# Performance work log

Hardware: AMD Instinct MI355X
Metric: run time of the kernel (lower is better)

Reference implementation:

```python
import jax, jax.numpy as jnp
import numpy as np

ROPE_BASE = 10000.0


def _rope_tables(m, d, dtype):
    # theta_i = 10000 ** (-2*(i-1)/d), i = 0..d/2-1 (faithful to the source's i-1)
    i = jnp.arange(d // 2, dtype=jnp.float32)
    theta = ROPE_BASE ** (-2.0 * (i - 1.0) / d)
    ang = jnp.arange(m, dtype=jnp.float32)[:, None] * theta[None, :]  # [m, d/2]
    return jnp.cos(ang).astype(dtype), jnp.sin(ang).astype(dtype)


def _rope(x, cos, sin):
    # x: [..., m, d]; row-vector times rotation matrix R[pos]:
    # out_2i = x_2i*cos + x_{2i+1}*sin ; out_{2i+1} = -x_2i*sin + x_{2i+1}*cos
    xp = x.reshape(x.shape[:-1] + (x.shape[-1] // 2, 2))
    xe, xo = xp[..., 0], xp[..., 1]
    oe = xe * cos + xo * sin
    oo = -xe * sin + xo * cos
    return jnp.stack([oe, oo], axis=-1).reshape(x.shape)


def setup_inputs() -> dict:
    key = jax.random.key(0)
    ks = jax.random.split(key, 6)
    B, M, D, H = 4, 2048, 512, 8
    s = 0.02
    return {
        "x": jax.random.normal(ks[0], (B, M, D), jnp.float32),
        "wq": jax.random.normal(ks[1], (H, D, D), jnp.float32) * s,
        "wk": jax.random.normal(ks[2], (H, D, D), jnp.float32) * s,
        "wv": jax.random.normal(ks[3], (H, D, D), jnp.float32) * s,
        "w_out": jax.random.normal(ks[4], (D, H * D), jnp.float32) * s,
        "b_out": jnp.zeros((D,), jnp.float32),
    }


def reference(x, wq, wk, wv, w_out, b_out):
    B, M, D = x.shape
    H = wq.shape[0]
    cos, sin = _rope_tables(M, D, x.dtype)
    # per-head projections (torch Linear: y = x @ W.T)
    q = jnp.einsum('bmd,hed->bhme', x, wq)
    k = jnp.einsum('bmd,hed->bhme', x, wk)
    v = jnp.einsum('bmd,hed->bhme', x, wv)
    qr = _rope(q, cos, sin)
    kr = _rope(k, cos, sin)
    scale = 1.0 / jnp.sqrt(jnp.asarray(D, x.dtype))
    scores = jnp.einsum('bhme,bhne->bhmn', qr, kr) * scale
    causal = jnp.tril(jnp.ones((M, M), bool))
    scores = jnp.where(causal, scores, jnp.asarray(-jnp.inf, scores.dtype))
    attn = jax.nn.softmax(scores, axis=-1)
    o = jnp.einsum('bhmn,bhne->bhme', attn, v)
    # concat heads on last dim (head order preserved), then output linear
    o = o.transpose(0, 2, 1, 3).reshape(B, M, H * D)
    y = jnp.einsum('bmf,df->bmd', o, w_out) + b_out
    return y  # dropout is identity in eval mode
```

## Files before the change

kernel.cpp:

```cpp
#include <hip/hip_runtime.h>
#include <hip/hip_bf16.h>
#include <math.h>


typedef __attribute__((ext_vector_type(8))) __bf16 bf16x8;
typedef __attribute__((ext_vector_type(4))) __bf16 bf16x4;
typedef __attribute__((ext_vector_type(4))) float f32x4;

#define MFMA16(a, b, c) __builtin_amdgcn_mfma_f32_16x16x32_bf16((a), (b), (c), 0, 0, 0)

__device__ __forceinline__ void g2l16(const void* g, void* l) {
  __builtin_amdgcn_global_load_lds((const __attribute__((address_space(1))) void*)g,
                                   (__attribute__((address_space(3))) void*)l, 16, 0, 0);
}

__global__ void prep_k(const float* __restrict__ x, const float* __restrict__ wq,
                       const float* __restrict__ wk, const float* __restrict__ wv,
                       const float* __restrict__ wo,
                       __bf16* __restrict__ xb, __bf16* __restrict__ wqb,
                       __bf16* __restrict__ wkb, __bf16* __restrict__ wvb,
                       __bf16* __restrict__ wob,
                       float* __restrict__ ct, float* __restrict__ st) {
  int i = blockIdx.x * 256 + threadIdx.x;
  if (i < 3145728) {
    const float* src;
    __bf16* dst;
    int off = i;
    if (i < 1048576) { src = x; dst = xb; }
    else if (i < 1572864) { src = wq; dst = wqb; off = i - 1048576; }
    else if (i < 2097152) { src = wk; dst = wkb; off = i - 1572864; }
    else if (i < 2621440) { src = wv; dst = wvb; off = i - 2097152; }
    else { src = wo; dst = wob; off = i - 2621440; }
    float4 f = reinterpret_cast<const float4*>(src)[off];
    bf16x4 o;
    o.x = (__bf16)f.x; o.y = (__bf16)f.y; o.z = (__bf16)f.z; o.w = (__bf16)f.w;
    reinterpret_cast<bf16x4*>(dst)[off] = o;
  } else {
    int idx = i - 3145728;
    int m = idx >> 8, j = idx & 255;
    float e = (-2.0f * ((float)j - 1.0f) / 512.0f) * 13.287712379549449f;
    float theta = exp2f(e);
    float ang = (float)m * theta;
    float s, c;
    sincosf(ang, &s, &c);
    ct[idx] = c;
    st[idx] = s;
  }
}

__global__ __launch_bounds__(256, 2) void qkv_gemm_k(
    const __bf16* __restrict__ Xb,
    const __bf16* __restrict__ Wqb, const __bf16* __restrict__ Wkb, const __bf16* __restrict__ Wvb,
    const float* __restrict__ ct, const float* __restrict__ st,
    __bf16* __restrict__ Q, __bf16* __restrict__ K, __bf16* __restrict__ VT,
    int G, int lg, int h0) {
  const int z = blockIdx.z;
  const int which = z >> lg, hl = z & (G - 1);
  const int h = h0 + hl;
  const __bf16* W = (which == 0 ? Wqb : which == 1 ? Wkb : Wvb) + (size_t)h * 262144;

  const int mbase = blockIdx.x * 128;
  const int nbase = blockIdx.y * 128;

  __shared__ alignas(16) __bf16 As[128 * 64];
  __shared__ alignas(16) __bf16 Bs[128 * 64];

  const int tid = threadIdx.x;
  const int lane = tid & 63, wid = tid >> 6;
  const int wr = wid >> 1, wc = wid & 1;
  const int l15 = lane & 15, l4 = lane >> 4;

  f32x4 acc[4][4];
#pragma unroll
  for (int i = 0; i < 4; i++)
#pragma unroll
    for (int j = 0; j < 4; j++) acc[i][j] = f32x4{0.f, 0.f, 0.f, 0.f};

  for (int kt = 0; kt < 8; ++kt) {
    const int kb = kt * 64;
#pragma unroll
    for (int i = 0; i < 4; i++) {
      int chunk = i * 256 + tid;
      int row = chunk >> 3, col = (chunk & 7) * 8;
      g2l16(Xb + (size_t)(mbase + row) * 512 + kb + col, As + (i * 256 + (tid & ~63)) * 8);
    }
#pragma unroll
    for (int i = 0; i < 4; i++) {
      int chunk = i * 256 + tid;
      int row = chunk >> 3, col = (chunk & 7) * 8;
      g2l16(W + (size_t)(nbase + row) * 512 + kb + col, Bs + (i * 256 + (tid & ~63)) * 8);
    }
    __syncthreads();
#pragma unroll
    for (int kk = 0; kk < 2; ++kk) {
      bf16x8 a[4], b[4];
#pragma unroll
      for (int i = 0; i < 4; i++)
        a[i] = *reinterpret_cast<const bf16x8*>(As + (wr * 64 + i * 16 + l15) * 64 + kk * 32 + l4 * 8);
#pragma unroll
      for (int j = 0; j < 4; j++)
        b[j] = *reinterpret_cast<const bf16x8*>(Bs + (wc * 64 + j * 16 + l15) * 64 + kk * 32 + l4 * 8);
#pragma unroll
      for (int i = 0; i < 4; i++)
#pragma unroll
        for (int j = 0; j < 4; j++) acc[i][j] = MFMA16(a[i], b[j], acc[i][j]);
    }
    __syncthreads();
  }

  if (which == 2) {
    const int b_ = mbase >> 11;
    const int mloc = mbase & 2047;
    __bf16* Tgw = VT + (size_t)(b_ * G + hl) * 512 * 2048;
#pragma unroll
    for (int i = 0; i < 4; i++) {
#pragma unroll
      for (int j = 0; j < 4; j++) {
        const int col = nbase + wc * 64 + j * 16 + l15;
        const int m0 = mloc + wr * 64 + i * 16 + l4 * 4;
        bf16x4 pk;
        pk.x = (__bf16)acc[i][j][0];
        pk.y = (__bf16)acc[i][j][1];
        pk.z = (__bf16)acc[i][j][2];
        pk.w = (__bf16)acc[i][j][3];
        *reinterpret_cast<bf16x4*>(&Tgw[(size_t)col * 2048 + m0]) = pk;
      }
    }
  } else {
    __bf16* Out = which ? K : Q;
#pragma unroll
    for (int i = 0; i < 4; i++) {
#pragma unroll
      for (int j = 0; j < 4; j++) {
        const int col = nbase + wc * 64 + j * 16 + l15;
#pragma unroll
        for (int r = 0; r < 4; r++) {
          const int rowg = mbase + wr * 64 + i * 16 + l4 * 4 + r;
          const int b_ = rowg >> 11, m = rowg & 2047;
          float v = acc[i][j][r];
          float pv = __shfl_xor(v, 1, 64);
          float c = ct[m * 256 + (col >> 1)];
          float s = st[m * 256 + (col >> 1)];
          v = (col & 1) ? (v * c - pv * s) : (v * c + pv * s);
          Out[(size_t)((b_ * G + hl) * 2048 + m) * 512 + col] = (__bf16)v;
        }
      }
    }
  }
}

__global__ __launch_bounds__(512) void flash_attn_k(
    const __bf16* __restrict__ Q, const __bf16* __restrict__ K, const __bf16* __restrict__ VT,
    __bf16* __restrict__ O0, int G, int lg) {
  const int bhN = 4 * G;
  const int L = blockIdx.x + 16 * blockIdx.y;
  const int half = L / (8 * bhN);
  const int r_ = L % (8 * bhN);
  const int bh = r_ % bhN;
  const int p_ = r_ / bhN;
  const int qblk = half ? (15 - p_) : p_;
  const int b = bh >> lg, hl = bh & (G - 1);
  const int tid = threadIdx.x, lane = tid & 63, wid = tid >> 6;
  const int l15 = lane & 15, l4 = lane >> 4;
  const int qw = qblk * 128 + wid * 16;

  __shared__ alignas(16) __bf16 Ks[32 * 512];
  __shared__ alignas(16) __bf16 Vts[512 * 32];
  __shared__ alignas(16) __bf16 Ps[8][16 * 32];

  const __bf16* Qg = Q + ((size_t)bh * 2048 + qw) * 512;
  const __bf16* Kg = K + (size_t)bh * 2048 * 512;
  const __bf16* Tg = VT + (size_t)bh * 512 * 2048;

  bf16x8 qf[16];
#pragma unroll
  for (int c = 0; c < 16; c++)
    qf[c] = *reinterpret_cast<const bf16x8*>(Qg + l15 * 512 + c * 32 + l4 * 8);

  f32x4 acc[32];
#pragma unroll
  for (int n = 0; n < 32; n++) acc[n] = f32x4{0.f, 0.f, 0.f, 0.f};
  float mrow[4] = {-INFINITY, -INFINITY, -INFINITY, -INFINITY};
  float lrow[4] = {0.f, 0.f, 0.f, 0.f};

  const float scale = 0.04419417382415922f;
  const int ntiles = qblk * 4 + 4;

  for (int kt = 0; kt < ntiles; ++kt) {
    const int kb = kt * 32;
#pragma unroll
    for (int i = 0; i < 4; i++) {
      int chunk = i * 512 + tid;
      int row = chunk >> 6, c16 = chunk & 63;
      g2l16(Kg + (size_t)(kb + row) * 512 + ((c16 ^ (row & 7)) << 3),
            Ks + (i * 512 + (tid & ~63)) * 8);
    }
#pragma unroll
    for (int i = 0; i < 4; i++) {
      int chunk = i * 512 + tid;
      int row = chunk >> 2, c4 = chunk & 3;
      g2l16(Tg + (size_t)row * 2048 + kb + ((c4 ^ ((row >> 1) & 3)) << 3),
            Vts + (i * 512 + (tid & ~63)) * 8);
    }
    __syncthreads();

    f32x4 sv0 = f32x4{0.f, 0.f, 0.f, 0.f}, sv1 = f32x4{0.f, 0.f, 0.f, 0.f};
#pragma unroll
    for (int c = 0; c < 16; c++) {
      const int off = c * 32 + l4 * 8;
      const int r0 = l15, r1 = 16 + l15;
      bf16x8 b0 = *reinterpret_cast<const bf16x8*>(Ks + r0 * 512 + (off ^ ((r0 & 7) << 3)));
      bf16x8 b1 = *reinterpret_cast<const bf16x8*>(Ks + r1 * 512 + (off ^ ((r1 & 7) << 3)));
      sv0 = MFMA16(qf[c], b0, sv0);
      sv1 = MFMA16(qf[c], b1, sv1);
    }

    float mx[4];
#pragma unroll
    for (int r = 0; r < 4; r++) {
      const int qg = qw + l4 * 4 + r;
      float s0 = sv0[r] * scale;
      float s1 = sv1[r] * scale;
      if (kb + l15 > qg) s0 = -INFINITY;
      if (kb + 16 + l15 > qg) s1 = -INFINITY;
      sv0[r] = s0; sv1[r] = s1;
      float m_ = fmaxf(s0, s1);
      m_ = fmaxf(m_, __shfl_xor(m_, 1, 64));
      m_ = fmaxf(m_, __shfl_xor(m_, 2, 64));
      m_ = fmaxf(m_, __shfl_xor(m_, 4, 64));
      m_ = fmaxf(m_, __shfl_xor(m_, 8, 64));
      mx[r] = m_;
    }
    bool need = (mx[0] > mrow[0] + 8.f) || (mx[1] > mrow[1] + 8.f) ||
                (mx[2] > mrow[2] + 8.f) || (mx[3] > mrow[3] + 8.f);
    if (__any(need)) {
      float alpha[4];
#pragma unroll
      for (int r = 0; r < 4; r++) {
        float mn = fmaxf(mrow[r], mx[r]);
        alpha[r] = __expf(mrow[r] - mn);
        lrow[r] *= alpha[r];
        mrow[r] = mn;
      }
#pragma unroll
      for (int n = 0; n < 32; n++) {
#pragma unroll
        for (int r = 0; r < 4; r++) acc[n][r] *= alpha[r];
      }
    }
#pragma unroll
    for (int r = 0; r < 4; r++) {
      float p0 = __expf(sv0[r] - mrow[r]);
      float p1 = __expf(sv1[r] - mrow[r]);
      float rs = p0 + p1;
      rs += __shfl_xor(rs, 1, 64);
      rs += __shfl_xor(rs, 2, 64);
      rs += __shfl_xor(rs, 4, 64);
      rs += __shfl_xor(rs, 8, 64);
      lrow[r] += rs;
      __bf16* P = &Ps[wid][0];
      P[(l4 * 4 + r) * 32 + l15] = (__bf16)p0;
      P[(l4 * 4 + r) * 32 + 16 + l15] = (__bf16)p1;
    }
    bf16x8 pf = *reinterpret_cast<const bf16x8*>(&Ps[wid][0] + l15 * 32 + l4 * 8);
#pragma unroll
    for (int n = 0; n < 32; n++) {
      const int row = n * 16 + l15;
      bf16x8 vb = *reinterpret_cast<const bf16x8*>(Vts + row * 32 + ((l4 * 8) ^ (((row >> 1) & 3) << 3)));
      acc[n] = MFMA16(pf, vb, acc[n]);
    }
    __syncthreads();
  }

#pragma unroll
  for (int r = 0; r < 4; r++) {
    const int qg = qw + l4 * 4 + r;
    const float inv = 1.0f / lrow[r];
    __bf16* Og = O0 + ((size_t)(b * 2048 + qg) * (512 * G) + hl * 512);
#pragma unroll
    for (int n = 0; n < 32; n++) Og[n * 16 + l15] = (__bf16)(acc[n][r] * inv);
  }
}

__global__ __launch_bounds__(512) void flashB_k(
    const __bf16* __restrict__ Q, const __bf16* __restrict__ K, const __bf16* __restrict__ VT,
    __bf16* __restrict__ O0, __bf16* __restrict__ O1, float2* __restrict__ Ml,
    int G, int lg) {
  const int bhN = 4 * G;
  const int L = blockIdx.x;
  const int bh = L % bhN;
  const int s_ = L / bhN;
  const int ks = (s_ < 16) ? 0 : 1;
  const int qblk = ks ? (31 - s_) : s_;
  const int hn = 2 * qblk + 2;
  const int kt0 = ks * hn, kt1 = kt0 + hn;
  const int b = bh >> lg, hl = bh & (G - 1);
  const int tid = threadIdx.x, lane = tid & 63, wid = tid >> 6;
  const int l15 = lane & 15, l4 = lane >> 4;
  const int qw = qblk * 128 + wid * 16;

  __shared__ alignas(16) __bf16 Ks[32 * 512];
  __shared__ alignas(16) __bf16 Vts[512 * 32];
  __shared__ alignas(16) __bf16 Ps[8][16 * 40];

  const __bf16* Qg = Q + ((size_t)bh * 2048 + qw) * 512;
  const __bf16* Kg = K + (size_t)bh * 2048 * 512;
  const __bf16* Tg = VT + (size_t)bh * 512 * 2048;

  bf16x8 qf[16];
#pragma unroll
  for (int c = 0; c < 16; c++)
    qf[c] = *reinterpret_cast<const bf16x8*>(Qg + l15 * 512 + c * 32 + l4 * 8);

  f32x4 acc[32];
#pragma unroll
  for (int n = 0; n < 32; n++) acc[n] = f32x4{0.f, 0.f, 0.f, 0.f};
  float mrow[4] = {-INFINITY, -INFINITY, -INFINITY, -INFINITY};
  float lrow[4] = {0.f, 0.f, 0.f, 0.f};

  const float scale = 0.04419417382415922f;

  auto stageK = [&](int kt2) {
#pragma unroll
    for (int i = 0; i < 4; i++) {
      int chunk = i * 512 + tid;
      int row = chunk >> 6, c16 = chunk & 63;
      g2l16(Kg + (size_t)(kt2 * 32 + row) * 512 + ((c16 ^ (row & 7)) << 3),
            Ks + (i * 512 + (tid & ~63)) * 8);
    }
  };
  auto stageV = [&](int kt2) {
#pragma unroll
    for (int i = 0; i < 4; i++) {
      int chunk = i * 512 + tid;
      int row = chunk >> 2, c4 = chunk & 3;
      g2l16(Tg + (size_t)row * 2048 + kt2 * 32 + ((c4 ^ ((row >> 1) & 3)) << 3),
            Vts + (i * 512 + (tid & ~63)) * 8);
    }
  };

  stageK(kt0);

  for (int kt = kt0; kt < kt1; ++kt) {
    const int kb = kt * 32;
    __syncthreads();
    stageV(kt);

    f32x4 sv0 = f32x4{0.f, 0.f, 0.f, 0.f}, sv1 = f32x4{0.f, 0.f, 0.f, 0.f};
#pragma unroll
    for (int c = 0; c < 16; c++) {
      const int off = c * 32 + l4 * 8;
      const int r0 = l15, r1 = 16 + l15;
      bf16x8 b0 = *reinterpret_cast<const bf16x8*>(Ks + r0 * 512 + (off ^ ((r0 & 7) << 3)));
      bf16x8 b1 = *reinterpret_cast<const bf16x8*>(Ks + r1 * 512 + (off ^ ((r1 & 7) << 3)));
      sv0 = MFMA16(qf[c], b0, sv0);
      sv1 = MFMA16(qf[c], b1, sv1);
    }

    float mx[4];
#pragma unroll
    for (int r = 0; r < 4; r++) {
      const int qg = qw + l4 * 4 + r;
      float s0 = sv0[r] * scale;
      float s1 = sv1[r] * scale;
      if (kb + l15 > qg) s0 = -INFINITY;
      if (kb + 16 + l15 > qg) s1 = -INFINITY;
      sv0[r] = s0; sv1[r] = s1;
      float m_ = fmaxf(s0, s1);
      m_ = fmaxf(m_, __shfl_xor(m_, 1, 64));
      m_ = fmaxf(m_, __shfl_xor(m_, 2, 64));
      m_ = fmaxf(m_, __shfl_xor(m_, 4, 64));
      m_ = fmaxf(m_, __shfl_xor(m_, 8, 64));
      mx[r] = m_;
    }
    bool need = (mx[0] > mrow[0] + 8.f) || (mx[1] > mrow[1] + 8.f) ||
                (mx[2] > mrow[2] + 8.f) || (mx[3] > mrow[3] + 8.f);
    if (__any(need)) {
      float alpha[4];
#pragma unroll
      for (int r = 0; r < 4; r++) {
        float mn = fmaxf(mrow[r], mx[r]);
        alpha[r] = __expf(mrow[r] - mn);
        lrow[r] *= alpha[r];
        mrow[r] = mn;
      }
#pragma unroll
      for (int n = 0; n < 32; n++) {
#pragma unroll
        for (int r = 0; r < 4; r++) acc[n][r] *= alpha[r];
      }
    }
#pragma unroll
    for (int r = 0; r < 4; r++) {
      float p0 = __expf(sv0[r] - mrow[r]);
      float p1 = __expf(sv1[r] - mrow[r]);
      float rs = p0 + p1;
      rs += __shfl_xor(rs, 1, 64);
      rs += __shfl_xor(rs, 2, 64);
      rs += __shfl_xor(rs, 4, 64);
      rs += __shfl_xor(rs, 8, 64);
      lrow[r] += rs;
      __bf16* P = &Ps[wid][0];
      P[(l4 * 4 + r) * 40 + l15] = (__bf16)p0;
      P[(l4 * 4 + r) * 40 + 16 + l15] = (__bf16)p1;
    }

    __syncthreads();
    if (kt + 1 < kt1) stageK(kt + 1);

    bf16x8 pf = *reinterpret_cast<const bf16x8*>(&Ps[wid][0] + l15 * 40 + l4 * 8);
#pragma unroll
    for (int n = 0; n < 32; n++) {
      const int row = n * 16 + l15;
      bf16x8 vb = *reinterpret_cast<const bf16x8*>(Vts + row * 32 + ((l4 * 8) ^ (((row >> 1) & 3) << 3)));
      acc[n] = MFMA16(pf, vb, acc[n]);
    }
  }

  __bf16* Osel = ks ? O1 : O0;
#pragma unroll
  for (int r = 0; r < 4; r++) {
    const int qg = qw + l4 * 4 + r;
    const float inv = 1.0f / lrow[r];
    __bf16* Og = Osel + ((size_t)(b * 2048 + qg) * (512 * G) + hl * 512);
#pragma unroll
    for (int n = 0; n < 32; n++) Og[n * 16 + l15] = (__bf16)(acc[n][r] * inv);
    if (l15 == 0) Ml[ks * bhN * 2048 + bh * 2048 + qg] = make_float2(mrow[r], lrow[r]);
  }
}

__global__ void merge_k(__bf16* __restrict__ O0, const __bf16* __restrict__ O1,
                        const float2* __restrict__ Ml, int G, int lg, int n8) {
  int idx = blockIdx.x * 256 + threadIdx.x;
  if (idx >= n8) return;
  const int bhN = 4 * G;
  size_t flat = (size_t)idx * 8;
  int rowG = (int)(flat >> 9);
  int hl = rowG & (G - 1);
  int bm = rowG >> lg;
  int b = bm >> 11, m = bm & 2047;
  int bh = b * G + hl;
  float2 ml0 = Ml[bh * 2048 + m];
  float2 ml1 = Ml[bhN * 2048 + bh * 2048 + m];
  float mm = fmaxf(ml0.x, ml1.x);
  float w0 = __expf(ml0.x - mm) * ml0.y;
  bool h1 = (ml1.y > 0.f);
  float w1 = h1 ? __expf(ml1.x - mm) * ml1.y : 0.f;
  float inv = 1.f / (w0 + w1);
  float a0 = w0 * inv, a1 = w1 * inv;
  bf16x8 v0 = *reinterpret_cast<const bf16x8*>(O0 + flat);
  bf16x8 out;
  if (h1) {
    bf16x8 v1 = *reinterpret_cast<const bf16x8*>(O1 + flat);
#pragma unroll
    for (int j = 0; j < 8; j++) out[j] = (__bf16)(a0 * (float)v0[j] + a1 * (float)v1[j]);
  } else {
#pragma unroll
    for (int j = 0; j < 8; j++) out[j] = (__bf16)(a0 * (float)v0[j]);
  }
  *reinterpret_cast<bf16x8*>(O0 + flat) = out;
}

__global__ __launch_bounds__(256) void out_gemm_k(
    const __bf16* __restrict__ A, const __bf16* __restrict__ Wo,
    const float* __restrict__ bias, float* __restrict__ Y, int G, int first) {
  const int AS = 512 * G;
  const int mbase = blockIdx.x * 128, nbase = blockIdx.y * 64;
  __shared__ alignas(16) __bf16 As[128 * 64];
  __shared__ alignas(16) __bf16 Bs[64 * 64];
  const int tid = threadIdx.x;
  const int lane = tid & 63, wid = tid >> 6;
  const int wr = wid >> 1, wc = wid & 1;
  const int l15 = lane & 15, l4 = lane >> 4;

  f32x4 acc[4][2];
#pragma unroll
  for (int i = 0; i < 4; i++)
#pragma unroll
    for (int j = 0; j < 2; j++) acc[i][j] = f32x4{0.f, 0.f, 0.f, 0.f};

  const int nkt = 8 * G;
  for (int kt = 0; kt < nkt; ++kt) {
    const int kb = kt * 64;
#pragma unroll
    for (int i = 0; i < 4; i++) {
      int chunk = i * 256 + tid;
      int row = chunk >> 3, col = (chunk & 7) * 8;
      g2l16(A + (size_t)(mbase + row) * AS + kb + col, As + (i * 256 + (tid & ~63)) * 8);
    }
#pragma unroll
    for (int i = 0; i < 2; i++) {
      int chunk = i * 256 + tid;
      int row = chunk >> 3, col = (chunk & 7) * 8;
      g2l16(Wo + (size_t)(nbase + row) * 4096 + kb + col, Bs + (i * 256 + (tid & ~63)) * 8);
    }
    __syncthreads();
#pragma unroll
    for (int kk = 0; kk < 2; ++kk) {
      bf16x8 a[4], b[2];
#pragma unroll
      for (int i = 0; i < 4; i++)
        a[i] = *reinterpret_cast<const bf16x8*>(As + (wr * 64 + i * 16 + l15) * 64 + kk * 32 + l4 * 8);
#pragma unroll
      for (int j = 0; j < 2; j++)
        b[j] = *reinterpret_cast<const bf16x8*>(Bs + (wc * 32 + j * 16 + l15) * 64 + kk * 32 + l4 * 8);
#pragma unroll
      for (int i = 0; i < 4; i++)
#pragma unroll
        for (int j = 0; j < 2; j++) acc[i][j] = MFMA16(a[i], b[j], acc[i][j]);
    }
    __syncthreads();
  }

#pragma unroll
  for (int i = 0; i < 4; i++) {
#pragma unroll
    for (int j = 0; j < 2; j++) {
      const int col = nbase + wc * 32 + j * 16 + l15;
#pragma unroll
      for (int r = 0; r < 4; r++) {
        const int row = mbase + wr * 64 + i * 16 + l4 * 4 + r;
        float prev = first ? bias[col] : Y[(size_t)row * 512 + col];
        Y[(size_t)row * 512 + col] = prev + acc[i][j][r];
      }
    }
  }
}

extern "C" void kernel_launch(void* const* d_in, const int* in_sizes, int n_in,
                              void* d_out, int out_size, void* d_ws, size_t ws_size,
                              hipStream_t stream) {
  (void)in_sizes; (void)n_in; (void)out_size;
  const float* x = (const float*)d_in[0];
  const float* wq = (const float*)d_in[1];
  const float* wk = (const float*)d_in[2];
  const float* wv = (const float*)d_in[3];
  const float* wo = (const float*)d_in[4];
  const float* bo = (const float*)d_in[5];
  float* y = (float*)d_out;

  char* base = (char*)d_ws;
  size_t off = 0;
  auto alloc = [&](size_t bytes) -> void* {
    void* p = base + off;
    off += (bytes + 255) & ~(size_t)255;
    return p;
  };
  __bf16* xb = (__bf16*)alloc((size_t)8192 * 512 * 2);
  __bf16* wqb = (__bf16*)alloc((size_t)8 * 512 * 512 * 2);
  __bf16* wkb = (__bf16*)alloc((size_t)8 * 512 * 512 * 2);
  __bf16* wvb = (__bf16*)alloc((size_t)8 * 512 * 512 * 2);
  __bf16* wob = (__bf16*)alloc((size_t)512 * 4096 * 2);
  float* ct = (float*)alloc((size_t)2048 * 256 * 4);
  float* st = (float*)alloc((size_t)2048 * 256 * 4);
  const size_t persist = off;

  int G = 0, lg = 0;
  for (int g = 8, l = 3; g >= 1; g >>= 1, --l) {
    size_t T = ((size_t)g * 4 * 2048 * 512 * 2 + 255) & ~(size_t)255;
    if (persist + 4 * T <= ws_size) { G = g; lg = l; break; }
  }
  if (G == 0) return;

  const int bhN = 4 * G;
  size_t T = ((size_t)G * 4 * 2048 * 512 * 2 + 255) & ~(size_t)255;
  size_t mlBytes = ((size_t)2 * bhN * 2048 * sizeof(float2) + 255) & ~(size_t)255;
  bool SPLIT = (G >= 2) && (persist + 5 * T + mlBytes <= ws_size);

  __bf16* Qb = (__bf16*)(base + persist);
  __bf16* Kb = (__bf16*)(base + persist + T);
  __bf16* VTb = (__bf16*)(base + persist + 2 * T);
  __bf16* Ob = (__bf16*)(base + persist + 3 * T);
  __bf16* O1b = SPLIT ? (__bf16*)(base + persist + 4 * T) : Ob;
  float2* Mlb = SPLIT ? (float2*)(base + persist + 5 * T) : (float2*)(base + persist);

  prep_k<<<14336, 256, 0, stream>>>(x, wq, wk, wv, wo, xb, wqb, wkb, wvb, wob, ct, st);

  const int n8 = bhN * 2048 * 64;
  for (int h0 = 0; h0 < 8; h0 += G) {
    qkv_gemm_k<<<dim3(64, 4, 3 * G), 256, 0, stream>>>(xb, wqb, wkb, wvb, ct, st,
                                                       Qb, Kb, VTb, G, lg, h0);
    if (SPLIT) {
      flashB_k<<<dim3(32 * bhN), 512, 0, stream>>>(Qb, Kb, VTb, Ob, O1b, Mlb, G, lg);
      merge_k<<<(n8 + 255) / 256, 256, 0, stream>>>(Ob, O1b, Mlb, G, lg, n8);
    } else {
      flash_attn_k<<<dim3(16, bhN), 512, 0, stream>>>(Qb, Kb, VTb, Ob, G, lg);
    }
    out_gemm_k<<<dim3(64, 8), 256, 0, stream>>>(Ob, wob + h0 * 512, bo, y, G, h0 == 0);
  }
}
```

Before: 629.4 us.

## Fuse split-KV merge into output projection GEMM via per-row weights

Replaces the elementwise merge kernel, which read both partial outputs and wrote the combined result back, with a small kernel that computes per-row combine weights. The output GEMM's A-tile load now reads both partial outputs and blends them in registers before writing to LDS. This removes a full read-modify-write pass over the attention output. In exchange, the GEMM loads twice the A data per tile through plain global loads instead of async loads. It also changes the running-max init to a finite value and guards against division by a zero row sum.

```diff
diff --git a/kernel.cpp b/kernel.cpp
--- a/kernel.cpp
+++ b/kernel.cpp
@@ -315,7 +315,7 @@
   f32x4 acc[32];
 #pragma unroll
   for (int n = 0; n < 32; n++) acc[n] = f32x4{0.f, 0.f, 0.f, 0.f};
-  float mrow[4] = {-INFINITY, -INFINITY, -INFINITY, -INFINITY};
+  float mrow[4] = {-1e30f, -1e30f, -1e30f, -1e30f};
   float lrow[4] = {0.f, 0.f, 0.f, 0.f};
 
   const float scale = 0.04419417382415922f;
@@ -421,7 +421,7 @@
 #pragma unroll
   for (int r = 0; r < 4; r++) {
     const int qg = qw + l4 * 4 + r;
-    const float inv = 1.0f / lrow[r];
+    const float inv = (lrow[r] > 0.f) ? (1.0f / lrow[r]) : 0.f;
     __bf16* Og = Osel + ((size_t)(b * 2048 + qg) * (512 * G) + hl * 512);
 #pragma unroll
     for (int n = 0; n < 32; n++) Og[n * 16 + l15] = (__bf16)(acc[n][r] * inv);
@@ -429,36 +429,105 @@
   }
 }
 
-__global__ void merge_k(__bf16* __restrict__ O0, const __bf16* __restrict__ O1,
-                        const float2* __restrict__ Ml, int G, int lg, int n8) {
+__global__ void weights_k(const float2* __restrict__ Ml, float2* __restrict__ Wm,
+                          int G, int nrow) {
   int idx = blockIdx.x * 256 + threadIdx.x;
-  if (idx >= n8) return;
+  if (idx >= nrow) return;
   const int bhN = 4 * G;
-  size_t flat = (size_t)idx * 8;
-  int rowG = (int)(flat >> 9);
-  int hl = rowG & (G - 1);
-  int bm = rowG >> lg;
-  int b = bm >> 11, m = bm & 2047;
-  int bh = b * G + hl;
-  float2 ml0 = Ml[bh * 2048 + m];
-  float2 ml1 = Ml[bhN * 2048 + bh * 2048 + m];
+  float2 ml0 = Ml[idx];
+  float2 ml1 = Ml[bhN * 2048 + idx];
   float mm = fmaxf(ml0.x, ml1.x);
   float w0 = __expf(ml0.x - mm) * ml0.y;
   bool h1 = (ml1.y > 0.f);
   float w1 = h1 ? __expf(ml1.x - mm) * ml1.y : 0.f;
   float inv = 1.f / (w0 + w1);
-  float a0 = w0 * inv, a1 = w1 * inv;
-  bf16x8 v0 = *reinterpret_cast<const bf16x8*>(O0 + flat);
-  bf16x8 out;
-  if (h1) {
-    bf16x8 v1 = *reinterpret_cast<const bf16x8*>(O1 + flat);
-#pragma unroll
-    for (int j = 0; j < 8; j++) out[j] = (__bf16)(a0 * (float)v0[j] + a1 * (float)v1[j]);
-  } else {
-#pragma unroll
-    for (int j = 0; j < 8; j++) out[j] = (__bf16)(a0 * (float)v0[j]);
-  }
-  *reinterpret_cast<bf16x8*>(O0 + flat) = out;
+  Wm[idx] = make_float2(w0 * inv, h1 ? w1 * inv : 0.f);
+}
+
+__global__ __launch_bounds__(256) void out_gemm_f_k(
+    const __bf16* __restrict__ O0, const __bf16* __restrict__ O1,
+    const float2* __restrict__ Wm, const __bf16* __restrict__ Wo,
+    const float* __restrict__ bias, float* __restrict__ Y, int G, int lg, int first) {
+  const int AS = 512 * G;
+  const int mbase = blockIdx.x * 128, nbase = blockIdx.y * 64;
+  __shared__ alignas(16) __bf16 As[128 * 64];
+  __shared__ alignas(16) __bf16 Bs[64 * 64];
+  const int tid = threadIdx.x;
+  const int lane = tid & 63, wid = tid >> 6;
+  const int wr = wid >> 1, wc = wid & 1;
+  const int l15 = lane & 15, l4 = lane >> 4;
+
+  f32x4 acc[4][2];
+#pragma unroll
+  for (int i = 0; i < 4; i++)
+#pragma unroll
+    for (int j = 0; j < 2; j++) acc[i][j] = f32x4{0.f, 0.f, 0.f, 0.f};
+
+  const int nkt = 8 * G;
+  for (int kt = 0; kt < nkt; ++kt) {
+    const int kb = kt * 64;
+    const int hl = kb >> 9;
+    bf16x8 av[4];
+    int chk[4];
+#pragma unroll
+    for (int i = 0; i < 4; i++) {
+      int chunk = i * 256 + tid;
+      chk[i] = chunk;
+      int row = chunk >> 3, col = (chunk & 7) * 8;
+      int g = mbase + row;
+      int m = g & 2047, b_ = g >> 11;
+      float2 w = Wm[(b_ * G + hl) * 2048 + m];
+      bf16x8 v0 = *reinterpret_cast<const bf16x8*>(O0 + (size_t)g * AS + kb + col);
+      bf16x8 v1 = *reinterpret_cast<const bf16x8*>(O1 + (size_t)g * AS + kb + col);
+      bf16x8 o;
+      const bool use1 = (w.y > 0.f);
+#pragma unroll
+      for (int j = 0; j < 8; j++) {
+        float t = use1 ? (w.y * (float)v1[j]) : 0.f;
+        o[j] = (__bf16)(w.x * (float)v0[j] + t);
+      }
+      av[i] = o;
+    }
+#pragma unroll
+    for (int i = 0; i < 2; i++) {
+      int chunk = i * 256 + tid;
+      int row = chunk >> 3, col = (chunk & 7) * 8;
+      g2l16(Wo + (size_t)(nbase + row) * 4096 + kb + col, Bs + (i * 256 + (tid & ~63)) * 8);
+    }
+#pragma unroll
+    for (int i = 0; i < 4; i++)
+      *reinterpret_cast<bf16x8*>(As + chk[i] * 8) = av[i];
+    __syncthreads();
+#pragma unroll
+    for (int kk = 0; kk < 2; ++kk) {
+      bf16x8 a[4], b[2];
+#pragma unroll
+      for (int i = 0; i < 4; i++)
+        a[i] = *reinterpret_cast<const bf16x8*>(As + (wr * 64 + i * 16 + l15) * 64 + kk * 32 + l4 * 8);
+#pragma unroll
+      for (int j = 0; j < 2; j++)
+        b[j] = *reinterpret_cast<const bf16x8*>(Bs + (wc * 32 + j * 16 + l15) * 64 + kk * 32 + l4 * 8);
+#pragma unroll
+      for (int i = 0; i < 4; i++)
+#pragma unroll
+        for (int j = 0; j < 2; j++) acc[i][j] = MFMA16(a[i], b[j], acc[i][j]);
+    }
+    __syncthreads();
+  }
+
+#pragma unroll
+  for (int i = 0; i < 4; i++) {
+#pragma unroll
+    for (int j = 0; j < 2; j++) {
+      const int col = nbase + wc * 32 + j * 16 + l15;
+#pragma unroll
+      for (int r = 0; r < 4; r++) {
+        const int row = mbase + wr * 64 + i * 16 + l4 * 4 + r;
+        float prev = first ? bias[col] : Y[(size_t)row * 512 + col];
+        Y[(size_t)row * 512 + col] = prev + acc[i][j][r];
+      }
+    }
+  }
 }
 
 __global__ __launch_bounds__(256) void out_gemm_k(
@@ -565,7 +634,8 @@
   const int bhN = 4 * G;
   size_t T = ((size_t)G * 4 * 2048 * 512 * 2 + 255) & ~(size_t)255;
   size_t mlBytes = ((size_t)2 * bhN * 2048 * sizeof(float2) + 255) & ~(size_t)255;
-  bool SPLIT = (G >= 2) && (persist + 5 * T + mlBytes <= ws_size);
+  size_t wmBytes = ((size_t)bhN * 2048 * sizeof(float2) + 255) & ~(size_t)255;
+  bool SPLIT = (G >= 2) && (persist + 5 * T + mlBytes + wmBytes <= ws_size);
 
   __bf16* Qb = (__bf16*)(base + persist);
   __bf16* Kb = (__bf16*)(base + persist + T);
@@ -573,19 +643,22 @@
   __bf16* Ob = (__bf16*)(base + persist + 3 * T);
   __bf16* O1b = SPLIT ? (__bf16*)(base + persist + 4 * T) : Ob;
   float2* Mlb = SPLIT ? (float2*)(base + persist + 5 * T) : (float2*)(base + persist);
+  float2* Wmb = SPLIT ? (float2*)(base + persist + 5 * T + mlBytes) : (float2*)(base + persist);
 
   prep_k<<<14336, 256, 0, stream>>>(x, wq, wk, wv, wo, xb, wqb, wkb, wvb, wob, ct, st);
 
-  const int n8 = bhN * 2048 * 64;
+  const int nrow = bhN * 2048;
   for (int h0 = 0; h0 < 8; h0 += G) {
     qkv_gemm_k<<<dim3(64, 4, 3 * G), 256, 0, stream>>>(xb, wqb, wkb, wvb, ct, st,
                                                        Qb, Kb, VTb, G, lg, h0);
     if (SPLIT) {
       flashB_k<<<dim3(32 * bhN), 512, 0, stream>>>(Qb, Kb, VTb, Ob, O1b, Mlb, G, lg);
-      merge_k<<<(n8 + 255) / 256, 256, 0, stream>>>(Ob, O1b, Mlb, G, lg, n8);
+      weights_k<<<(nrow + 255) / 256, 256, 0, stream>>>(Mlb, Wmb, G, nrow);
+      out_gemm_f_k<<<dim3(64, 8), 256, 0, stream>>>(Ob, O1b, Wmb, wob + h0 * 512, bo, y,
+                                                    G, lg, h0 == 0);
     } else {
       flash_attn_k<<<dim3(16, bhN), 512, 0, stream>>>(Qb, Kb, VTb, Ob, G, lg);
-    }
-    out_gemm_k<<<dim3(64, 8), 256, 0, stream>>>(Ob, wob + h0 * 512, bo, y, G, h0 == 0);
-  }
-}
+      out_gemm_k<<<dim3(64, 8), 256, 0, stream>>>(Ob, wob + h0 * 512, bo, y, G, h0 == 0);
+    }
+  }
+}
```

New measurement: 714.2 us. 1.13x slower.
